# Kernel optimization log

Measured on AMD Instinct MI355X. Metric: run time of the kernel, lower is better.

The kernel has to match this reference:

```python
import jax, jax.numpy as jnp
import numpy as np
from jax import lax

BATCH = 64
SEQ = 80
VOCAB = 10000
EMBED = 100
UNITS = 2048


def setup_inputs() -> dict:
    key = jax.random.key(0)
    ks = jax.random.split(key, 10)
    s = lambda *sh: 1.0 / np.sqrt(sh[0])
    inputs = jax.random.randint(ks[0], (BATCH, SEQ), 0, VOCAB, dtype=jnp.int32)
    emb = jax.random.normal(ks[1], (VOCAB, EMBED), jnp.float32) * 0.05
    Wx0 = jax.random.normal(ks[2], (EMBED, UNITS), jnp.float32) * s(EMBED)
    Wh0 = jax.random.normal(ks[3], (UNITS, UNITS), jnp.float32) * s(UNITS)
    b0 = jnp.zeros((UNITS,), jnp.float32)
    Wx1 = jax.random.normal(ks[4], (UNITS, UNITS), jnp.float32) * s(UNITS)
    Wh1 = jax.random.normal(ks[5], (UNITS, UNITS), jnp.float32) * s(UNITS)
    b1 = jnp.zeros((UNITS,), jnp.float32)
    Wo = jax.random.normal(ks[6], (UNITS, 1), jnp.float32) * s(UNITS)
    bo = jnp.zeros((1,), jnp.float32)
    return {"inputs": inputs, "emb": emb, "Wx0": Wx0, "Wh0": Wh0, "b0": b0,
            "Wx1": Wx1, "Wh1": Wh1, "b1": b1, "Wo": Wo, "bo": bo}


def reference(inputs, emb, Wx0, Wh0, b0, Wx1, Wh1, b1, Wo, bo):
    # Embedding lookup: [B, T, E]
    x = emb[inputs]
    B = inputs.shape[0]
    units = Wh0.shape[0]
    h0 = jnp.zeros((B, units), x.dtype)
    h1 = jnp.zeros((B, units), x.dtype)

    def step(carry, xt):
        h0, h1 = carry
        # SimpleRNNCell: h = tanh(x @ Wx + h_prev @ Wh + b); dropout off (inference)
        h0 = jnp.tanh(xt @ Wx0 + h0 @ Wh0 + b0)
        h1 = jnp.tanh(h0 @ Wx1 + h1 @ Wh1 + b1)
        return (h0, h1), None

    (h0, h1), _ = lax.scan(step, (h0, h1), jnp.swapaxes(x, 0, 1))  # scan over T
    return jax.nn.sigmoid(h1 @ Wo + bo)  # [B, 1]
```

## Files before the change

kernel.cpp:

```cpp
#include <hip/hip_runtime.h>

#define BB 64
#define TT 80
#define EE 100
#define UU 2048
#define NWG 192

typedef float f32x4 __attribute__((ext_vector_type(4)));
typedef unsigned int u32x4 __attribute__((ext_vector_type(4)));
typedef __bf16 bf16x8 __attribute__((ext_vector_type(8)));
typedef unsigned long long u64;

#define XPROJ_OFF 0u
#define WPACK_OFF 20971520u
#define H0_OFF    46137344u
#define H1_OFF    50331648u
#define PX_OFF    54525952u
#define H1F_OFF   58720256u
#define BAR_OFF   59244544u
#define WS_NEEDED 59293696u
#define ZERO_U4   822272

#define LDS_BYTES 147968

__device__ __forceinline__ unsigned short f2bf(float f) {
  unsigned int u = __float_as_uint(f);
  u += 0x7fffu + ((u >> 16) & 1u);
  return (unsigned short)(u >> 16);
}
__device__ __forceinline__ float bf2f(unsigned short h) {
  return __uint_as_float(((unsigned int)h) << 16);
}
__device__ __forceinline__ u64 pack4(float a, float b, float c, float d) {
  return (u64)f2bf(a) | ((u64)f2bf(b) << 16) | ((u64)f2bf(c) << 32) | ((u64)f2bf(d) << 48);
}
__device__ __forceinline__ bf16x8 u2b(u32x4 u) {
  union { u32x4 q; bf16x8 b; } x; x.q = u; return x.b;
}
__device__ __forceinline__ f32x4 u2f(u32x4 u) {
  union { u32x4 q; f32x4 f; } x; x.q = u; return x.f;
}

__device__ __forceinline__ void st_flag(int* p, int v) {
  asm volatile("global_store_dword %0, %1, off sc0 sc1" :: "v"(p), "v"(v) : "memory");
}
__device__ __forceinline__ int ld_flag(const int* p) {
  int r;
  asm volatile("global_load_dword %0, %1, off sc0 sc1\n\ts_waitcnt vmcnt(0)"
               : "=v"(r) : "v"(p) : "memory");
  return r;
}

__global__ void zero_init(u32x4* __restrict__ p, int n) {
  u32x4 z = {0u, 0u, 0u, 0u};
  for (int i = blockIdx.x * blockDim.x + threadIdx.x; i < n; i += gridDim.x * blockDim.x)
    p[i] = z;
}

__global__ __launch_bounds__(256) void pack_weights(
    const float* __restrict__ Wh0, const float* __restrict__ Wx1,
    const float* __restrict__ Wh1, unsigned short* __restrict__ wpack) {
  __shared__ float tile[32][33];
  const int bb = blockIdx.x;
  const int L = bb >> 7;
  const int rest = bb & 127;
  const int wl = rest >> 1;
  const int kh = rest & 1;
  const float* src = (L == 0) ? Wh0 : (L == 1) ? Wx1 : Wh1;
  const int tid = threadIdx.x;
  const int kr = tid >> 3, cqr = tid & 7;
  const int c = tid >> 7;
  const int lane = (tid >> 1) & 63;
  const int jh = (tid & 1) << 2;
  const int l16 = lane & 15, lq = lane >> 4;
  const size_t wg = (size_t)(L << 6) + wl;

  for (int kc = 0; kc < 32; ++kc) {
    const int kq = (kh << 1) + (kc >> 4);
    const int kt = kc & 15;
    const int k0 = (kh << 10) + (kc << 5);
    float4 v = *(const float4*)&src[(size_t)(k0 + kr) * 2048u + (wl << 5) + (cqr << 2)];
    tile[kr][cqr * 4 + 0] = v.x;
    tile[kr][cqr * 4 + 1] = v.y;
    tile[kr][cqr * 4 + 2] = v.z;
    tile[kr][cqr * 4 + 3] = v.w;
    __syncthreads();
    ushort4 o;
    o.x = f2bf(tile[lq * 8 + jh + 0][c * 16 + l16]);
    o.y = f2bf(tile[lq * 8 + jh + 1][c * 16 + l16]);
    o.z = f2bf(tile[lq * 8 + jh + 2][c * 16 + l16]);
    o.w = f2bf(tile[lq * 8 + jh + 3][c * 16 + l16]);
    size_t doff = (wg << 16) + ((size_t)kq << 14) + ((size_t)kt << 10) + (c << 9) + (lane << 3) + jh;
    *(ushort4*)&wpack[doff] = o;
    __syncthreads();
  }
}

__global__ __launch_bounds__(256) void xproj_kernel(
    const int* __restrict__ inputs, const float* __restrict__ emb,
    const float* __restrict__ Wx0, const float* __restrict__ b0,
    unsigned short* __restrict__ xp) {
  __shared__ float X[64][100];
  __shared__ float Wl[100][64];
  __shared__ int idx[64];
  const int t = blockIdx.y, ut = blockIdx.x, tid = threadIdx.x;
  if (tid < 64) idx[tid] = inputs[tid * TT + t];
  __syncthreads();
  for (int i = tid; i < 6400; i += 256) {
    int b = i / 100, e = i - b * 100;
    X[b][e] = emb[(size_t)idx[b] * EE + e];
  }
  for (int i = tid; i < 6400; i += 256) {
    int e = i >> 6, u = i & 63;
    Wl[e][u] = Wx0[(size_t)e * UU + (ut << 6) + u];
  }
  __syncthreads();
  const int ul = tid & 63, bg = tid >> 6;
  float accv[16];
  const float bias = b0[(ut << 6) + ul];
#pragma unroll
  for (int q = 0; q < 16; ++q) accv[q] = bias;
  for (int e4 = 0; e4 < 100; e4 += 4) {
    float w0 = Wl[e4 + 0][ul], w1 = Wl[e4 + 1][ul], w2 = Wl[e4 + 2][ul], w3 = Wl[e4 + 3][ul];
#pragma unroll
    for (int q = 0; q < 16; ++q) {
      float4 x4 = *(const float4*)&X[bg * 16 + q][e4];
      accv[q] += w0 * x4.x + w1 * x4.y + w2 * x4.z + w3 * x4.w;
    }
  }
  unsigned short* dst = xp + ((size_t)t * 64u) * 2048u + (ut << 6);
#pragma unroll
  for (int q = 0; q < 16; ++q) dst[(size_t)(bg * 16 + q) * 2048u + ul] = f2bf(accv[q]);
}

__global__ __launch_bounds__(256, 1) void rnn_persistent(
    const unsigned short* __restrict__ xproj, const unsigned short* __restrict__ wpack,
    unsigned short* __restrict__ h0b, unsigned short* __restrict__ h1b,
    float* __restrict__ px, float* __restrict__ h1f,
    const float* __restrict__ b1, int* __restrict__ bar) {
  extern __shared__ char smem[];
  unsigned short* wlds = (unsigned short*)smem;
  float* red = (float*)(smem + 131072);
  const int wg = blockIdx.x, tid = threadIdx.x;
  const int wave = tid >> 6, lane = tid & 63;
  const int layer = wg >> 6, wl = wg & 63;
  const int l16 = lane & 15, lq = lane >> 4;
  const int colb = wl << 5;

  {
    const u32x4* srcp = (const u32x4*)(wpack + ((size_t)wg << 16));
    u32x4* dstp = (u32x4*)smem;
    for (int i = tid; i < 8192; i += 256) dstp[i] = srcp[i];
  }
  __syncthreads();

  const unsigned short* wbase = wlds + (wave << 14) + (lane << 3);
  const int aoff = l16 * 2048 + (wave << 9) + (lq << 3);
  const int r0 = tid >> 3, cq = tid & 7;
  const int r1 = r0 + 32;

  const int gA = (layer == 2) ? 1 : 0;
  const int gB = (layer == 0) ? 1 : 2;

  for (int t = 0; t < 80; ++t) {
    const int tgtA = (layer == 0) ? t : (t + 1);
    const int tgtB = (layer == 0) ? (t - 15) : (layer == 1) ? (t - 7) : t;

    if (wave == 0) {
      if (tgtA > 0) {
        const int* p = bar + (((gA << 6) + lane) << 6);
        int guard = 0;
        while (ld_flag(p) < tgtA) {
          __builtin_amdgcn_s_sleep(1);
          if (++guard > (1 << 18)) break;
        }
      }
    } else if (wave == 1) {
      if (tgtB > 0) {
        const int* p = bar + (((gB << 6) + lane) << 6);
        int guard = 0;
        while (ld_flag(p) < tgtB) {
          __builtin_amdgcn_s_sleep(1);
          if (++guard > (1 << 18)) break;
        }
      }
    }
    __syncthreads();
    if ((t & 7) == 0) {
      asm volatile("buffer_inv sc1" ::: "memory");
    }

    const unsigned short* Abuf =
        (layer == 0) ? (h0b + (size_t)((t + 15) & 15) * 131072u)
      : (layer == 1) ? (h0b + (size_t)(t & 15) * 131072u)
                     : (h1b + (size_t)((t + 15) & 15) * 131072u);
    const unsigned short* ap0 = Abuf + aoff;
    const unsigned short* ap1 = ap0 + 16 * 2048;
    const unsigned short* ap2 = ap0 + 32 * 2048;
    const unsigned short* ap3 = ap0 + 48 * 2048;

    u32x4 pxq0, pxq1;
    if (layer == 2) {
      const float* pxs = px + (size_t)(t & 7) * 131072u;
      const float* pp0 = pxs + r0 * 2048 + colb + (cq << 2);
      const float* pp1 = pxs + r1 * 2048 + colb + (cq << 2);
      asm volatile("global_load_dwordx4 %0, %2, off\n\t"
                   "global_load_dwordx4 %1, %3, off"
                   : "=v"(pxq0), "=v"(pxq1) : "v"(pp0), "v"(pp1) : "memory");
    }

    u32x4 Asl[8][4];
    f32x4 c00 = {0,0,0,0}, c01 = {0,0,0,0}, c10 = {0,0,0,0}, c11 = {0,0,0,0};
    f32x4 c20 = {0,0,0,0}, c21 = {0,0,0,0}, c30 = {0,0,0,0}, c31 = {0,0,0,0};

#define ISSUE(sl, koff) \
    asm volatile("global_load_dwordx4 %0, %4, off offset:" #koff "\n\t" \
                 "global_load_dwordx4 %1, %5, off offset:" #koff "\n\t" \
                 "global_load_dwordx4 %2, %6, off offset:" #koff "\n\t" \
                 "global_load_dwordx4 %3, %7, off offset:" #koff \
                 : "=v"(Asl[sl][0]), "=v"(Asl[sl][1]), "=v"(Asl[sl][2]), "=v"(Asl[sl][3]) \
                 : "v"(ap0), "v"(ap1), "v"(ap2), "v"(ap3) : "memory")

    ISSUE(0, 0);   ISSUE(1, 64);  ISSUE(2, 128); ISSUE(3, 192);
    ISSUE(4, 256); ISSUE(5, 320); ISSUE(6, 384); ISSUE(7, 448);

    bf16x8 cb0 = *(const bf16x8*)(wbase);
    bf16x8 cb1 = *(const bf16x8*)(wbase + 512);

#define MFMA8(sl) \
    c00 = __builtin_amdgcn_mfma_f32_16x16x32_bf16(u2b(Asl[sl][0]), cb0, c00, 0, 0, 0); \
    c10 = __builtin_amdgcn_mfma_f32_16x16x32_bf16(u2b(Asl[sl][1]), cb0, c10, 0, 0, 0); \
    c20 = __builtin_amdgcn_mfma_f32_16x16x32_bf16(u2b(Asl[sl][2]), cb0, c20, 0, 0, 0); \
    c30 = __builtin_amdgcn_mfma_f32_16x16x32_bf16(u2b(Asl[sl][3]), cb0, c30, 0, 0, 0); \
    c01 = __builtin_amdgcn_mfma_f32_16x16x32_bf16(u2b(Asl[sl][0]), cb1, c01, 0, 0, 0); \
    c11 = __builtin_amdgcn_mfma_f32_16x16x32_bf16(u2b(Asl[sl][1]), cb1, c11, 0, 0, 0); \
    c21 = __builtin_amdgcn_mfma_f32_16x16x32_bf16(u2b(Asl[sl][2]), cb1, c21, 0, 0, 0); \
    c31 = __builtin_amdgcn_mfma_f32_16x16x32_bf16(u2b(Asl[sl][3]), cb1, c31, 0, 0, 0)

#define KTI(kt, vN, koff) { \
    asm volatile("s_waitcnt vmcnt(" #vN ")" ::: "memory"); \
    __builtin_amdgcn_sched_barrier(0); \
    bf16x8 nb0 = *(const bf16x8*)(wbase + (kt + 1) * 1024); \
    bf16x8 nb1 = *(const bf16x8*)(wbase + (kt + 1) * 1024 + 512); \
    MFMA8((kt) & 7); \
    ISSUE((kt) & 7, koff); \
    cb0 = nb0; cb1 = nb1; }

#define KTN(kt, vN) { \
    asm volatile("s_waitcnt vmcnt(" #vN ")" ::: "memory"); \
    __builtin_amdgcn_sched_barrier(0); \
    bf16x8 nb0 = cb0, nb1 = cb1; \
    if ((kt) < 15) { nb0 = *(const bf16x8*)(wbase + (kt + 1) * 1024); \
                     nb1 = *(const bf16x8*)(wbase + (kt + 1) * 1024 + 512); } \
    MFMA8((kt) & 7); \
    cb0 = nb0; cb1 = nb1; }

    KTI(0, 28, 512); KTI(1, 28, 576); KTI(2, 28, 640); KTI(3, 28, 704);
    KTI(4, 28, 768); KTI(5, 28, 832); KTI(6, 28, 896); KTI(7, 28, 960);
    KTN(8, 28); KTN(9, 24); KTN(10, 20); KTN(11, 16);
    KTN(12, 12); KTN(13, 8); KTN(14, 4); KTN(15, 0);

#undef ISSUE
#undef MFMA8
#undef KTI
#undef KTN

#define WRROW(cv, rg, cc) { int bi = ((rg)*16 + lq*4)*33 + (cc)*16 + l16; \
    rb[bi] = cv[0]; rb[bi+33] = cv[1]; rb[bi+66] = cv[2]; rb[bi+99] = cv[3]; }
#define ADROW(cv, rg, cc) { int bi = ((rg)*16 + lq*4)*33 + (cc)*16 + l16; \
    rb[bi] += cv[0]; rb[bi+33] += cv[1]; rb[bi+66] += cv[2]; rb[bi+99] += cv[3]; }
    if (wave < 2) {
      float* rb = red + wave * 2112;
      WRROW(c00, 0, 0); WRROW(c10, 1, 0); WRROW(c20, 2, 0); WRROW(c30, 3, 0);
      WRROW(c01, 0, 1); WRROW(c11, 1, 1); WRROW(c21, 2, 1); WRROW(c31, 3, 1);
    }
    __syncthreads();
    if (wave >= 2) {
      float* rb = red + (wave - 2) * 2112;
      ADROW(c00, 0, 0); ADROW(c10, 1, 0); ADROW(c20, 2, 0); ADROW(c30, 3, 0);
      ADROW(c01, 0, 1); ADROW(c11, 1, 1); ADROW(c21, 2, 1); ADROW(c31, 3, 1);
    }
    __syncthreads();
#undef WRROW
#undef ADROW

    {
      const int gc = colb + (cq << 2);
      auto do_item = [&](int r, u32x4 pxq) {
        const int c0 = cq << 2;
        float v0 = red[r * 33 + c0 + 0] + red[2112 + r * 33 + c0 + 0];
        float v1 = red[r * 33 + c0 + 1] + red[2112 + r * 33 + c0 + 1];
        float v2 = red[r * 33 + c0 + 2] + red[2112 + r * 33 + c0 + 2];
        float v3 = red[r * 33 + c0 + 3] + red[2112 + r * 33 + c0 + 3];
        const size_t ro = ((size_t)r << 11) + gc;
        if (layer == 0) {
          u64 xq = *(const u64*)(xproj + (size_t)t * 131072u + ro);
          v0 = tanhf(v0 + bf2f((unsigned short)(xq)));
          v1 = tanhf(v1 + bf2f((unsigned short)(xq >> 16)));
          v2 = tanhf(v2 + bf2f((unsigned short)(xq >> 32)));
          v3 = tanhf(v3 + bf2f((unsigned short)(xq >> 48)));
          u64 o = pack4(v0, v1, v2, v3);
          unsigned short* hp = h0b + (size_t)(t & 15) * 131072u + ro;
          asm volatile("global_store_dwordx2 %0, %1, off sc0 sc1" :: "v"(hp), "v"(o) : "memory");
        } else if (layer == 1) {
          float4 bq = *(const float4*)&b1[gc];
          f32x4 o4; o4[0] = v0 + bq.x; o4[1] = v1 + bq.y; o4[2] = v2 + bq.z; o4[3] = v3 + bq.w;
          float* pp = px + (size_t)(t & 7) * 131072u + ro;
          asm volatile("global_store_dwordx4 %0, %1, off sc0 sc1" :: "v"(pp), "v"(o4) : "memory");
        } else {
          f32x4 pxf = u2f(pxq);
          v0 = tanhf(v0 + pxf[0]);
          v1 = tanhf(v1 + pxf[1]);
          v2 = tanhf(v2 + pxf[2]);
          v3 = tanhf(v3 + pxf[3]);
          u64 o = pack4(v0, v1, v2, v3);
          unsigned short* hp = h1b + (size_t)(t & 15) * 131072u + ro;
          asm volatile("global_store_dwordx2 %0, %1, off sc0 sc1" :: "v"(hp), "v"(o) : "memory");
          if (t == 79) {
            f32x4 f4; f4[0] = v0; f4[1] = v1; f4[2] = v2; f4[3] = v3;
            *(f32x4*)&h1f[ro] = f4;
          }
        }
      };
      do_item(r0, pxq0);
      do_item(r1, pxq1);
    }
    asm volatile("s_waitcnt vmcnt(0)" ::: "memory");

    __syncthreads();
    if (tid == 0) st_flag(&bar[wg << 6], t + 1);
  }
}

__global__ __launch_bounds__(256) void out_kernel(
    const float* __restrict__ h1f, const float* __restrict__ Wo,
    const float* __restrict__ bo, float* __restrict__ out) {
  const int b = blockIdx.x, tid = threadIdx.x;
  const float* row = h1f + (size_t)b * 2048u;
  float p = 0.f;
  for (int u = tid; u < 2048; u += 256) p += row[u] * Wo[u];
#pragma unroll
  for (int off = 32; off > 0; off >>= 1) p += __shfl_down(p, off, 64);
  __shared__ float wsum[4];
  if ((tid & 63) == 0) wsum[tid >> 6] = p;
  __syncthreads();
  if (tid == 0) {
    float sth = wsum[0] + wsum[1] + wsum[2] + wsum[3] + bo[0];
    out[b] = 1.f / (1.f + __expf(-sth));
  }
}

extern "C" void kernel_launch(void* const* d_in, const int* in_sizes, int n_in,
                              void* d_out, int out_size, void* d_ws, size_t ws_size,
                              hipStream_t stream) {
  (void)in_sizes; (void)n_in; (void)out_size;
  if (ws_size < (size_t)WS_NEEDED) return;

  const int*   inputs = (const int*)d_in[0];
  const float* emb    = (const float*)d_in[1];
  const float* Wx0    = (const float*)d_in[2];
  const float* Wh0    = (const float*)d_in[3];
  const float* b0     = (const float*)d_in[4];
  const float* Wx1    = (const float*)d_in[5];
  const float* Wh1    = (const float*)d_in[6];
  const float* b1     = (const float*)d_in[7];
  const float* Wo     = (const float*)d_in[8];
  const float* bo     = (const float*)d_in[9];
  float* out = (float*)d_out;
  char* ws = (char*)d_ws;

  unsigned short* xproj = (unsigned short*)(ws + XPROJ_OFF);
  unsigned short* wpack = (unsigned short*)(ws + WPACK_OFF);
  unsigned short* h0b   = (unsigned short*)(ws + H0_OFF);
  unsigned short* h1b   = (unsigned short*)(ws + H1_OFF);
  float* px   = (float*)(ws + PX_OFF);
  float* h1f  = (float*)(ws + H1F_OFF);
  int*   bar  = (int*)(ws + BAR_OFF);

  (void)hipFuncSetAttribute((const void*)rnn_persistent,
                            hipFuncAttributeMaxDynamicSharedMemorySize, LDS_BYTES);

  zero_init<<<256, 256, 0, stream>>>((u32x4*)(ws + H0_OFF), ZERO_U4);
  pack_weights<<<384, 256, 0, stream>>>(Wh0, Wx1, Wh1, wpack);
  xproj_kernel<<<dim3(32, 80), 256, 0, stream>>>(inputs, emb, Wx0, b0, xproj);
  rnn_persistent<<<NWG, 256, LDS_BYTES, stream>>>(xproj, wpack, h0b, h1b, px, h1f, b1, bar);
  out_kernel<<<64, 256, 0, stream>>>(h1f, Wo, bo, out);
}
```

Measured before the change: 1.109 ms.

## Remap RNN workgroups across XCDs and store layer-1 partials in bf16

The persistent kernel now launches 256 workgroups and maps them to roles by XCD (blockIdx & 7). Layers 0 and 1 sit on the first four XCDs and layer 2 on the remaining four, and the 64 surplus workgroups exit at once. The aim is to keep producer and consumer groups on shared L2 domains and cut cross-XCD coherence traffic. The inter-layer partial sums (px) are also stored as bf16 instead of fp32, which halves that buffer's traffic and the workspace size but adds rounding error to layer 2's input.

```diff
diff --git a/kernel.cpp b/kernel.cpp
--- a/kernel.cpp
+++ b/kernel.cpp
@@ -4,7 +4,7 @@
 #define TT 80
 #define EE 100
 #define UU 2048
-#define NWG 192
+#define NWG 256
 
 typedef float f32x4 __attribute__((ext_vector_type(4)));
 typedef unsigned int u32x4 __attribute__((ext_vector_type(4)));
@@ -16,10 +16,10 @@
 #define H0_OFF    46137344u
 #define H1_OFF    50331648u
 #define PX_OFF    54525952u
-#define H1F_OFF   58720256u
-#define BAR_OFF   59244544u
-#define WS_NEEDED 59293696u
-#define ZERO_U4   822272
+#define H1F_OFF   56623104u
+#define BAR_OFF   57147392u
+#define WS_NEEDED 57196544u
+#define ZERO_U4   691200
 
 #define LDS_BYTES 147968
 
@@ -36,9 +36,6 @@
 }
 __device__ __forceinline__ bf16x8 u2b(u32x4 u) {
   union { u32x4 q; bf16x8 b; } x; x.q = u; return x.b;
-}
-__device__ __forceinline__ f32x4 u2f(u32x4 u) {
-  union { u32x4 q; f32x4 f; } x; x.q = u; return x.f;
 }
 
 __device__ __forceinline__ void st_flag(int* p, int v) {
@@ -73,7 +70,7 @@
   const int lane = (tid >> 1) & 63;
   const int jh = (tid & 1) << 2;
   const int l16 = lane & 15, lq = lane >> 4;
-  const size_t wg = (size_t)(L << 6) + wl;
+  const size_t rid = (size_t)(L << 6) + wl;
 
   for (int kc = 0; kc < 32; ++kc) {
     const int kq = (kh << 1) + (kc >> 4);
@@ -90,7 +87,7 @@
     o.y = f2bf(tile[lq * 8 + jh + 1][c * 16 + l16]);
     o.z = f2bf(tile[lq * 8 + jh + 2][c * 16 + l16]);
     o.w = f2bf(tile[lq * 8 + jh + 3][c * 16 + l16]);
-    size_t doff = (wg << 16) + ((size_t)kq << 14) + ((size_t)kt << 10) + (c << 9) + (lane << 3) + jh;
+    size_t doff = (rid << 16) + ((size_t)kq << 14) + ((size_t)kt << 10) + (c << 9) + (lane << 3) + jh;
     *(ushort4*)&wpack[doff] = o;
     __syncthreads();
   }
@@ -136,19 +133,30 @@
 __global__ __launch_bounds__(256, 1) void rnn_persistent(
     const unsigned short* __restrict__ xproj, const unsigned short* __restrict__ wpack,
     unsigned short* __restrict__ h0b, unsigned short* __restrict__ h1b,
-    float* __restrict__ px, float* __restrict__ h1f,
+    unsigned short* __restrict__ pxb, float* __restrict__ h1f,
     const float* __restrict__ b1, int* __restrict__ bar) {
+  const int wg = blockIdx.x, tid = threadIdx.x;
+  const int xcd = wg & 7, slot = wg >> 3;
+  int layer, wl;
+  if (xcd < 4) {
+    layer = slot >> 4;
+    wl = (xcd << 4) + (slot & 15);
+  } else {
+    if (slot >= 16) return;
+    layer = 2;
+    wl = ((xcd - 4) << 4) + (slot & 15);
+  }
+  const int rid = (layer << 6) + wl;
+
   extern __shared__ char smem[];
   unsigned short* wlds = (unsigned short*)smem;
   float* red = (float*)(smem + 131072);
-  const int wg = blockIdx.x, tid = threadIdx.x;
   const int wave = tid >> 6, lane = tid & 63;
-  const int layer = wg >> 6, wl = wg & 63;
   const int l16 = lane & 15, lq = lane >> 4;
   const int colb = wl << 5;
 
   {
-    const u32x4* srcp = (const u32x4*)(wpack + ((size_t)wg << 16));
+    const u32x4* srcp = (const u32x4*)(wpack + ((size_t)rid << 16));
     u32x4* dstp = (u32x4*)smem;
     for (int i = tid; i < 8192; i += 256) dstp[i] = srcp[i];
   }
@@ -199,13 +207,13 @@
     const unsigned short* ap2 = ap0 + 32 * 2048;
     const unsigned short* ap3 = ap0 + 48 * 2048;
 
-    u32x4 pxq0, pxq1;
+    u64 pxq0 = 0, pxq1 = 0;
     if (layer == 2) {
-      const float* pxs = px + (size_t)(t & 7) * 131072u;
-      const float* pp0 = pxs + r0 * 2048 + colb + (cq << 2);
-      const float* pp1 = pxs + r1 * 2048 + colb + (cq << 2);
-      asm volatile("global_load_dwordx4 %0, %2, off\n\t"
-                   "global_load_dwordx4 %1, %3, off"
+      const unsigned short* pxs = pxb + (size_t)(t & 7) * 131072u;
+      const unsigned short* pp0 = pxs + r0 * 2048 + colb + (cq << 2);
+      const unsigned short* pp1 = pxs + r1 * 2048 + colb + (cq << 2);
+      asm volatile("global_load_dwordx2 %0, %2, off\n\t"
+                   "global_load_dwordx2 %1, %3, off"
                    : "=v"(pxq0), "=v"(pxq1) : "v"(pp0), "v"(pp1) : "memory");
     }
 
@@ -286,7 +294,7 @@
 
     {
       const int gc = colb + (cq << 2);
-      auto do_item = [&](int r, u32x4 pxq) {
+      auto do_item = [&](int r, u64 pxq) {
         const int c0 = cq << 2;
         float v0 = red[r * 33 + c0 + 0] + red[2112 + r * 33 + c0 + 0];
         float v1 = red[r * 33 + c0 + 1] + red[2112 + r * 33 + c0 + 1];
@@ -304,15 +312,14 @@
           asm volatile("global_store_dwordx2 %0, %1, off sc0 sc1" :: "v"(hp), "v"(o) : "memory");
         } else if (layer == 1) {
           float4 bq = *(const float4*)&b1[gc];
-          f32x4 o4; o4[0] = v0 + bq.x; o4[1] = v1 + bq.y; o4[2] = v2 + bq.z; o4[3] = v3 + bq.w;
-          float* pp = px + (size_t)(t & 7) * 131072u + ro;
-          asm volatile("global_store_dwordx4 %0, %1, off sc0 sc1" :: "v"(pp), "v"(o4) : "memory");
+          u64 o = pack4(v0 + bq.x, v1 + bq.y, v2 + bq.z, v3 + bq.w);
+          unsigned short* pp = pxb + (size_t)(t & 7) * 131072u + ro;
+          asm volatile("global_store_dwordx2 %0, %1, off sc0 sc1" :: "v"(pp), "v"(o) : "memory");
         } else {
-          f32x4 pxf = u2f(pxq);
-          v0 = tanhf(v0 + pxf[0]);
-          v1 = tanhf(v1 + pxf[1]);
-          v2 = tanhf(v2 + pxf[2]);
-          v3 = tanhf(v3 + pxf[3]);
+          v0 = tanhf(v0 + bf2f((unsigned short)(pxq)));
+          v1 = tanhf(v1 + bf2f((unsigned short)(pxq >> 16)));
+          v2 = tanhf(v2 + bf2f((unsigned short)(pxq >> 32)));
+          v3 = tanhf(v3 + bf2f((unsigned short)(pxq >> 48)));
           u64 o = pack4(v0, v1, v2, v3);
           unsigned short* hp = h1b + (size_t)(t & 15) * 131072u + ro;
           asm volatile("global_store_dwordx2 %0, %1, off sc0 sc1" :: "v"(hp), "v"(o) : "memory");
@@ -328,7 +335,7 @@
     asm volatile("s_waitcnt vmcnt(0)" ::: "memory");
 
     __syncthreads();
-    if (tid == 0) st_flag(&bar[wg << 6], t + 1);
+    if (tid == 0) st_flag(&bar[rid << 6], t + 1);
   }
 }
 
@@ -373,7 +380,7 @@
   unsigned short* wpack = (unsigned short*)(ws + WPACK_OFF);
   unsigned short* h0b   = (unsigned short*)(ws + H0_OFF);
   unsigned short* h1b   = (unsigned short*)(ws + H1_OFF);
-  float* px   = (float*)(ws + PX_OFF);
+  unsigned short* pxb   = (unsigned short*)(ws + PX_OFF);
   float* h1f  = (float*)(ws + H1F_OFF);
   int*   bar  = (int*)(ws + BAR_OFF);
 
@@ -383,6 +390,6 @@
   zero_init<<<256, 256, 0, stream>>>((u32x4*)(ws + H0_OFF), ZERO_U4);
   pack_weights<<<384, 256, 0, stream>>>(Wh0, Wx1, Wh1, wpack);
   xproj_kernel<<<dim3(32, 80), 256, 0, stream>>>(inputs, emb, Wx0, b0, xproj);
-  rnn_persistent<<<NWG, 256, LDS_BYTES, stream>>>(xproj, wpack, h0b, h1b, px, h1f, b1, bar);
+  rnn_persistent<<<NWG, 256, LDS_BYTES, stream>>>(xproj, wpack, h0b, h1b, pxb, h1f, b1, bar);
   out_kernel<<<64, 256, 0, stream>>>(h1f, Wo, bo, out);
 }
```

New measurement: 1.117 ms. About the same (+0.8%).
